# Kernel optimization log

Hardware: AMD Instinct MI355X
Metric: run time of the kernel (lower is better)

## Reference

```python
import jax, jax.numpy as jnp
import numpy as np

N = 50000      # num nodes
E = 800000     # num edges (no self loops; added in reference like add_remaining_self_loops)
D = 64         # input_dim
H = 128        # hidden_dim
O = 32         # output_dim
EPS = 1.0      # epsilon (privacy)
ALPHA = 0.5
DELTA = 1.0


def setup_inputs() -> dict:
    key = jax.random.key(0)
    ks = jax.random.split(key, 8)
    x = jax.random.normal(ks[0], (N, D), dtype=jnp.float32)
    row = jax.random.randint(ks[1], (E,), 0, N, dtype=jnp.int32)
    off = jax.random.randint(ks[2], (E,), 1, N, dtype=jnp.int32)
    col = (row + off) % N  # guarantees row != col (no pre-existing self loops)
    edge_index = jnp.stack([row, col], axis=0)
    priv_mask = jax.random.bernoulli(ks[3], 0.5, (N,))
    W1 = jax.random.normal(ks[4], (D, H), dtype=jnp.float32) * (1.0 / np.sqrt(D))
    b1 = jnp.zeros((H,), dtype=jnp.float32)
    W2 = jax.random.normal(ks[5], (H, O), dtype=jnp.float32) * (1.0 / np.sqrt(H))
    b2 = jnp.zeros((O,), dtype=jnp.float32)
    return {"x": x, "edge_index": edge_index, "priv_mask": priv_mask,
            "W1": W1, "b1": b1, "W2": W2, "b2": b2}


def _gcn_norm(edge_index, num_nodes, dtype):
    # add_remaining_self_loops + symmetric normalization deg^-1/2[row]*deg^-1/2[col]
    loops = jnp.arange(num_nodes, dtype=edge_index.dtype)
    row = jnp.concatenate([edge_index[0], loops])
    col = jnp.concatenate([edge_index[1], loops])
    deg = jax.ops.segment_sum(jnp.ones(row.shape[0], dtype=dtype), row,
                              num_segments=num_nodes)
    dis = deg ** -0.5  # deg >= 1 thanks to self loops
    norm = dis[row] * dis[col]  # [E+N]
    return row, col, norm


def reference(x, edge_index, priv_mask, W1, b1, W2, b2):
    row, col, norm = _gcn_norm(edge_index, N, x.dtype)
    exp_eps = float(np.exp(EPS))

    # ---- conv1 (GConvDP with per-node bool priv_mask) ----
    x_j = x[row]                                   # [E+N, D] gather
    p = priv_mask[row].astype(x.dtype)[:, None]    # [E+N, 1]
    transformed = ((exp_eps + 1.0) * x_j - 1.0) * (DELTA / (exp_eps - 1.0)) + ALPHA
    msg = norm[:, None] * (p * transformed + (1.0 - p) * x_j)
    h = jax.ops.segment_sum(msg, col, num_segments=N)  # scatter-add aggregate

    h = jax.nn.relu(h @ W1 + b1)
    # F.dropout skipped: reference is deterministic (eval mode)

    # ---- conv2 (called with priv_mask=False, a Python scalar) ----
    # Literal torch semantics: p_j = False -> False*(...) = 0, ~False = -1,
    # so msg = norm * (-x_j).
    msg2 = -norm[:, None] * h[row]                 # [E+N, H]
    h2 = jax.ops.segment_sum(msg2, col, num_segments=N)

    return h2 @ W2 + b2
```

## Files before the change

kernel.cpp:

```cpp
#include <hip/hip_runtime.h>
#include <math.h>

#define C1 2.163953413738653f
#define C0 -0.081976706869326f


static __device__ __forceinline__ unsigned short f2bf(float f) {
    unsigned b = __float_as_uint(f);
    return (unsigned short)((b + 0x7FFFu + ((b >> 16) & 1u)) >> 16);
}
static __device__ __forceinline__ float bf2f(unsigned short u) {
    return __uint_as_float((unsigned)u << 16);
}

__global__ __launch_bounds__(1024) void k_hist2(const int* __restrict__ row,
                                                const int* __restrict__ col, int E, int chunk,
                                                int* __restrict__ hist) {
    __shared__ int hc[256], hr[256];
    int t = threadIdx.x, b = blockIdx.x;
    if (t < 256) { hc[t] = 0; hr[t] = 0; }
    __syncthreads();
    int lo = b * chunk, hi = min(E, lo + chunk);
    for (int i = lo + t; i < hi; i += 1024) {
        atomicAdd(&hc[col[i] >> 8], 1);
        atomicAdd(&hr[row[i] >> 8], 1);
    }
    __syncthreads();
    if (t < 256) {
        hist[t * 256 + b] = hc[t];
        hist[65536 + t * 256 + b] = hr[t];
    }
}

__global__ void k_scan_a(const int* __restrict__ cnt, int* __restrict__ excl,
                         int* __restrict__ bsum, int n) {
    __shared__ int s[256];
    int idx = blockIdx.x * 256 + threadIdx.x;
    int v = (idx < n) ? cnt[idx] : 0;
    s[threadIdx.x] = v;
    __syncthreads();
    for (int off = 1; off < 256; off <<= 1) {
        int t = (threadIdx.x >= off) ? s[threadIdx.x - off] : 0;
        __syncthreads();
        s[threadIdx.x] += t;
        __syncthreads();
    }
    if (idx < n) excl[idx] = s[threadIdx.x] - v;
    if (threadIdx.x == 255) bsum[blockIdx.x] = s[255];
}

__global__ __launch_bounds__(512) void k_scan_bc(int* __restrict__ excl,
                                                 const int* __restrict__ bsum) {
    __shared__ int s[512];
    int t = threadIdx.x, b = blockIdx.x;
    s[t] = (t < b) ? bsum[t] : 0;
    __syncthreads();
    for (int off = 256; off > 0; off >>= 1) {
        if (t < off) s[t] += s[t + off];
        __syncthreads();
    }
    if (t < 256) excl[b * 256 + t] += s[0];
}

__global__ __launch_bounds__(1024) void k_part(const int* __restrict__ row,
                                               const int* __restrict__ col, int E, int chunk,
                                               const int* __restrict__ shist,
                                               unsigned* __restrict__ cbuf,
                                               unsigned short* __restrict__ rbuf) {
    __shared__ int offc[256], offr[256];
    int t = threadIdx.x, b = blockIdx.x;
    if (t < 256) {
        offc[t] = shist[t * 256 + b];
        offr[t] = shist[65536 + t * 256 + b] - E;
    }
    __syncthreads();
    int lo = b * chunk, hi = min(E, lo + chunk);
    for (int i = lo + t; i < hi; i += 1024) {
        int r = row[i], c = col[i];
        int pc = atomicAdd(&offc[c >> 8], 1);
        cbuf[pc] = ((unsigned)c << 16) | (unsigned)r;
        int pr = atomicAdd(&offr[r >> 8], 1);
        rbuf[pr] = (unsigned short)r;
    }
}

__global__ __launch_bounds__(256) void k_build(const unsigned short* __restrict__ rbuf,
                                               const unsigned* __restrict__ cbuf,
                                               const int* __restrict__ shist,
                                               const int* __restrict__ priv,
                                               const float* __restrict__ x, int N, int E, int nbk,
                                               float* __restrict__ dis,
                                               unsigned short* __restrict__ xt,
                                               int* __restrict__ cntC, int* __restrict__ colStart,
                                               unsigned short* __restrict__ eSrc) {
    __shared__ int s1[256], s2[256], s3[256];
    int t = threadIdx.x;
    if ((int)blockIdx.x < nbk) {
        int b = blockIdx.x;
        s1[t] = 0;
        __syncthreads();
        int rs = shist[65536 + b * 256] - E;
        int re = shist[65536 + (b + 1) * 256] - E;
        for (int i = rs + t; i < re; i += 256) atomicAdd(&s1[rbuf[i] & 255], 1);
        __syncthreads();
        int node = b * 256 + t;
        float dv = rsqrtf((float)(s1[t] + 1));
        if (node < N) {
            dis[node] = dv;
            s2[t] = __float_as_int(dv);
            s3[t] = priv[node];
        } else { s2[t] = 0; s3[t] = 0; }
        __syncthreads();
        int base = b * 256;
        for (int i = t; i < 256 * 16; i += 256) {
            int ln = i >> 4;
            int n2 = base + ln;
            if (n2 >= N) continue;
            float d2 = __int_as_float(s2[ln]);
            int p = s3[ln];
            float4 v = ((const float4*)x)[(size_t)n2 * 16 + (i & 15)];
            float4 tr;
            tr.x = p ? fmaf(C1, v.x, C0) : v.x;
            tr.y = p ? fmaf(C1, v.y, C0) : v.y;
            tr.z = p ? fmaf(C1, v.z, C0) : v.z;
            tr.w = p ? fmaf(C1, v.w, C0) : v.w;
            ushort4 o;
            o.x = f2bf(d2 * tr.x); o.y = f2bf(d2 * tr.y);
            o.z = f2bf(d2 * tr.z); o.w = f2bf(d2 * tr.w);
            ((ushort4*)xt)[(size_t)n2 * 16 + (i & 15)] = o;
        }
    } else {
        int b = blockIdx.x - nbk;
        s1[t] = 0; s3[t] = 0;
        __syncthreads();
        int cs = shist[b * 256];
        int ce = shist[(b + 1) * 256];
        for (int i = cs + t; i < ce; i += 256) atomicAdd(&s1[(cbuf[i] >> 16) & 255], 1);
        __syncthreads();
        int v = s1[t];
        s2[t] = v;
        __syncthreads();
        for (int off = 1; off < 256; off <<= 1) {
            int u = (t >= off) ? s2[t - off] : 0;
            __syncthreads();
            s2[t] += u;
            __syncthreads();
        }
        int excl = s2[t] - v;
        int c = b * 256 + t;
        if (c < N) { cntC[c] = v; colStart[c] = cs + excl; }
        __syncthreads();
        s2[t] = excl;
        __syncthreads();
        for (int i = cs + t; i < ce; i += 256) {
            unsigned e = cbuf[i];
            int d = (e >> 16) & 255;
            int pos = cs + s2[d] + atomicAdd(&s3[d], 1);
            eSrc[pos] = (unsigned short)(e & 0xFFFFu);
        }
    }
}

__global__ __launch_bounds__(256) void k_gather1(const unsigned short* __restrict__ xt,
                                                 const unsigned short* __restrict__ eSrc,
                                                 const int* __restrict__ colStart,
                                                 const int* __restrict__ cntC,
                                                 const float* __restrict__ dis,
                                                 unsigned short* __restrict__ agg1b, int N) {
    int t = blockIdx.x * blockDim.x + threadIdx.x;
    int c = t >> 6, d = t & 63;
    if (c >= N) return;
    float s = bf2f(xt[(size_t)c * 64 + d]);
    int start = colStart[c], cnt = cntC[c];
    for (int base = 0; base < cnt; base += 64) {
        int m = min(cnt - base, 64);
        int ids = (d < m) ? (int)eSrc[start + base + d] : 0;
        int k = 0;
        for (; k + 8 <= m; k += 8) {
            int r0 = __shfl(ids, k),     r1 = __shfl(ids, k + 1);
            int r2 = __shfl(ids, k + 2), r3 = __shfl(ids, k + 3);
            int r4 = __shfl(ids, k + 4), r5 = __shfl(ids, k + 5);
            int r6 = __shfl(ids, k + 6), r7 = __shfl(ids, k + 7);
            float x0 = bf2f(xt[(size_t)r0 * 64 + d]);
            float x1 = bf2f(xt[(size_t)r1 * 64 + d]);
            float x2 = bf2f(xt[(size_t)r2 * 64 + d]);
            float x3 = bf2f(xt[(size_t)r3 * 64 + d]);
            float x4 = bf2f(xt[(size_t)r4 * 64 + d]);
            float x5 = bf2f(xt[(size_t)r5 * 64 + d]);
            float x6 = bf2f(xt[(size_t)r6 * 64 + d]);
            float x7 = bf2f(xt[(size_t)r7 * 64 + d]);
            s += x0; s += x1; s += x2; s += x3;
            s += x4; s += x5; s += x6; s += x7;
        }
        for (; k + 4 <= m; k += 4) {
            int r0 = __shfl(ids, k),     r1 = __shfl(ids, k + 1);
            int r2 = __shfl(ids, k + 2), r3 = __shfl(ids, k + 3);
            float x0 = bf2f(xt[(size_t)r0 * 64 + d]);
            float x1 = bf2f(xt[(size_t)r1 * 64 + d]);
            float x2 = bf2f(xt[(size_t)r2 * 64 + d]);
            float x3 = bf2f(xt[(size_t)r3 * 64 + d]);
            s += x0; s += x1; s += x2; s += x3;
        }
        for (; k < m; ++k) {
            int r = __shfl(ids, k);
            s += bf2f(xt[(size_t)r * 64 + d]);
        }
    }
    agg1b[(size_t)c * 64 + d] = f2bf(dis[c] * s);
}

__global__ __launch_bounds__(256) void k_mlp_fused(const unsigned short* __restrict__ agg1b,
                                                   const float* __restrict__ W1,
                                                   const float* __restrict__ b1,
                                                   const float* __restrict__ W2,
                                                   const float* __restrict__ dis,
                                                   unsigned short* __restrict__ hps, int N) {
    __shared__ float hidT[128 * 68];
    __shared__ float W2s[128 * 32];
    float* As = hidT;
    const int t = threadIdx.x;
    const int base = blockIdx.x * 64;

    for (int i = t * 4; i < 128 * 32; i += 1024)
        *(float4*)&W2s[i] = *(const float4*)&W2[i];

    {
        int kq = t & 15, mm = t >> 4;
        #pragma unroll
        for (int p = 0; p < 4; ++p) {
            int m = mm + p * 16;
            int node = base + m;
            if (node >= N) node = N - 1;
            ushort4 v = ((const ushort4*)agg1b)[(size_t)node * 16 + kq];
            As[(kq * 4 + 0) * 68 + m] = bf2f(v.x);
            As[(kq * 4 + 1) * 68 + m] = bf2f(v.y);
            As[(kq * 4 + 2) * 68 + m] = bf2f(v.z);
            As[(kq * 4 + 3) * 68 + m] = bf2f(v.w);
        }
    }
    __syncthreads();

    const int tn = t & 31;
    const int tm = t >> 5;
    float4 bv = *(const float4*)&b1[tn * 4];
    float acc[8][4];
    #pragma unroll
    for (int i = 0; i < 8; ++i) {
        acc[i][0] = bv.x; acc[i][1] = bv.y; acc[i][2] = bv.z; acc[i][3] = bv.w;
    }
    #pragma unroll 4
    for (int k = 0; k < 64; ++k) {
        float4 w  = *(const float4*)&W1[k * 128 + tn * 4];
        float4 a0 = *(const float4*)&As[k * 68 + tm * 8];
        float4 a1 = *(const float4*)&As[k * 68 + tm * 8 + 4];
        const float av[8] = {a0.x, a0.y, a0.z, a0.w, a1.x, a1.y, a1.z, a1.w};
        #pragma unroll
        for (int i = 0; i < 8; ++i) {
            acc[i][0] = fmaf(av[i], w.x, acc[i][0]);
            acc[i][1] = fmaf(av[i], w.y, acc[i][1]);
            acc[i][2] = fmaf(av[i], w.z, acc[i][2]);
            acc[i][3] = fmaf(av[i], w.w, acc[i][3]);
        }
    }
    __syncthreads();

    #pragma unroll
    for (int j = 0; j < 4; ++j)
        #pragma unroll
        for (int i = 0; i < 8; ++i)
            hidT[(tn * 4 + j) * 68 + tm * 8 + i] = fmaxf(acc[i][j], 0.f);
    __syncthreads();

    const int to  = t & 15;
    const int tm2 = t >> 4;
    float o0[4] = {0.f, 0.f, 0.f, 0.f};
    float o1[4] = {0.f, 0.f, 0.f, 0.f};
    #pragma unroll 4
    for (int kh = 0; kh < 128; ++kh) {
        float4 a = *(const float4*)&hidT[kh * 68 + tm2 * 4];
        float2 w = *(const float2*)&W2s[kh * 32 + to * 2];
        const float av[4] = {a.x, a.y, a.z, a.w};
        #pragma unroll
        for (int i = 0; i < 4; ++i) {
            o0[i] = fmaf(av[i], w.x, o0[i]);
            o1[i] = fmaf(av[i], w.y, o1[i]);
        }
    }
    #pragma unroll
    for (int i = 0; i < 4; ++i) {
        int node = base + tm2 * 4 + i;
        if (node < N) {
            float dv = dis[node];
            ushort2 o = make_ushort2(f2bf(o0[i] * dv), f2bf(o1[i] * dv));
            *(ushort2*)&hps[(size_t)node * 32 + to * 2] = o;
        }
    }
}

__global__ __launch_bounds__(256) void k_gather2(const unsigned short* __restrict__ hps,
                                                 const unsigned short* __restrict__ eSrc,
                                                 const int* __restrict__ colStart,
                                                 const int* __restrict__ cntC,
                                                 const float* __restrict__ dis,
                                                 const float* __restrict__ b2,
                                                 float* __restrict__ out, int N) {
    int t = blockIdx.x * blockDim.x + threadIdx.x;
    int c = t >> 5, j = t & 31;
    if (c >= N) return;
    float s = bf2f(hps[(size_t)c * 32 + j]);
    int start = colStart[c], cnt = cntC[c];
    for (int base = 0; base < cnt; base += 32) {
        int m = min(cnt - base, 32);
        int ids = (j < m) ? (int)eSrc[start + base + j] : 0;
        int k = 0;
        for (; k + 8 <= m; k += 8) {
            int r0 = __shfl(ids, k, 32),     r1 = __shfl(ids, k + 1, 32);
            int r2 = __shfl(ids, k + 2, 32), r3 = __shfl(ids, k + 3, 32);
            int r4 = __shfl(ids, k + 4, 32), r5 = __shfl(ids, k + 5, 32);
            int r6 = __shfl(ids, k + 6, 32), r7 = __shfl(ids, k + 7, 32);
            float h0 = bf2f(hps[(size_t)r0 * 32 + j]);
            float h1 = bf2f(hps[(size_t)r1 * 32 + j]);
            float h2 = bf2f(hps[(size_t)r2 * 32 + j]);
            float h3 = bf2f(hps[(size_t)r3 * 32 + j]);
            float h4 = bf2f(hps[(size_t)r4 * 32 + j]);
            float h5 = bf2f(hps[(size_t)r5 * 32 + j]);
            float h6 = bf2f(hps[(size_t)r6 * 32 + j]);
            float h7 = bf2f(hps[(size_t)r7 * 32 + j]);
            s += h0; s += h1; s += h2; s += h3;
            s += h4; s += h5; s += h6; s += h7;
        }
        for (; k + 4 <= m; k += 4) {
            int r0 = __shfl(ids, k, 32),     r1 = __shfl(ids, k + 1, 32);
            int r2 = __shfl(ids, k + 2, 32), r3 = __shfl(ids, k + 3, 32);
            float h0 = bf2f(hps[(size_t)r0 * 32 + j]);
            float h1 = bf2f(hps[(size_t)r1 * 32 + j]);
            float h2 = bf2f(hps[(size_t)r2 * 32 + j]);
            float h3 = bf2f(hps[(size_t)r3 * 32 + j]);
            s += h0; s += h1; s += h2; s += h3;
        }
        for (; k < m; ++k) {
            int r = __shfl(ids, k, 32);
            s += bf2f(hps[(size_t)r * 32 + j]);
        }
    }
    out[(size_t)c * 32 + j] = b2[j] - dis[c] * s;
}

extern "C" void kernel_launch(void* const* d_in, const int* in_sizes, int n_in,
                              void* d_out, int out_size, void* d_ws, size_t ws_size,
                              hipStream_t stream) {
    const float* x    = (const float*)d_in[0];
    const int*   ei   = (const int*)d_in[1];
    const int*   priv = (const int*)d_in[2];
    const float* W1   = (const float*)d_in[3];
    const float* b1   = (const float*)d_in[4];
    const float* W2   = (const float*)d_in[5];
    const float* b2   = (const float*)d_in[6];
    float* out = (float*)d_out;

    const int N = in_sizes[2];
    const int E = in_sizes[1] / 2;
    const int* row = ei;
    const int* col = ei + E;

    char* ws = (char*)d_ws;
    size_t off = 0;
    auto take = [&](size_t bytes) { char* p = ws + off; off = (off + bytes + 255) & ~(size_t)255; return p; };
    int*            hist     = (int*)           take((size_t)131072 * 4);
    int*            shist    = (int*)           take((size_t)131072 * 4);
    int*            bsum     = (int*)           take(512 * 4);
    unsigned*       cbuf     = (unsigned*)      take((size_t)E * 4);
    unsigned short* rbuf     = (unsigned short*)take((size_t)E * 2);
    float*          dis      = (float*)         take((size_t)N * 4);
    int*            cntC     = (int*)           take((size_t)N * 4);
    int*            colStart = (int*)           take((size_t)N * 4);
    unsigned short* eSrc     = (unsigned short*)take((size_t)E * 2);
    unsigned short* xt       = (unsigned short*)take((size_t)N * 64 * 2);
    unsigned short* agg1b    = (unsigned short*)take((size_t)N * 64 * 2);
    unsigned short* hps      = (unsigned short*)take((size_t)N * 32 * 2);
    (void)ws_size;

    const int chunk = (E + 255) / 256;
    const int nbk = (N + 255) / 256;

    k_hist2    <<<256, 1024, 0, stream>>>(row, col, E, chunk, hist);
    k_scan_a   <<<512, 256, 0, stream>>>(hist, shist, bsum, 131072);
    k_scan_bc  <<<512, 512, 0, stream>>>(shist, bsum);
    k_part     <<<256, 1024, 0, stream>>>(row, col, E, chunk, shist, cbuf, rbuf);
    k_build    <<<2 * nbk, 256, 0, stream>>>(rbuf, cbuf, shist, priv, x, N, E, nbk,
                                             dis, xt, cntC, colStart, eSrc);
    k_gather1  <<<((size_t)N * 64 + 255) / 256, 256, 0, stream>>>(xt, eSrc, colStart, cntC, dis, agg1b, N);
    k_mlp_fused<<<(N + 63) / 64, 256, 0, stream>>>(agg1b, W1, b1, W2, dis, hps, N);
    k_gather2  <<<((size_t)N * 32 + 255) / 256, 256, 0, stream>>>(hps, eSrc, colStart, cntC, dis, b2, out, N);
}
```

Before: 175.8 us.

## Use bf16 MFMA for fused MLP and fold scan fixup into consumers

```diff
diff --git a/kernel.cpp b/kernel.cpp
--- a/kernel.cpp
+++ b/kernel.cpp
@@ -4,6 +4,9 @@
 #define C1 2.163953413738653f
 #define C0 -0.081976706869326f
 
+
+typedef __attribute__((ext_vector_type(8))) short bf16x8;
+typedef __attribute__((ext_vector_type(4))) float f32x4;
 
 static __device__ __forceinline__ unsigned short f2bf(float f) {
     unsigned b = __float_as_uint(f);
@@ -15,7 +18,11 @@
 
 __global__ __launch_bounds__(1024) void k_hist2(const int* __restrict__ row,
                                                 const int* __restrict__ col, int E, int chunk,
-                                                int* __restrict__ hist) {
+                                                int* __restrict__ hist,
+                                                const float* __restrict__ W1,
+                                                const float* __restrict__ W2,
+                                                unsigned short* __restrict__ W1b,
+                                                unsigned short* __restrict__ W2b) {
     __shared__ int hc[256], hr[256];
     int t = threadIdx.x, b = blockIdx.x;
     if (t < 256) { hc[t] = 0; hr[t] = 0; }
@@ -29,6 +36,19 @@
     if (t < 256) {
         hist[t * 256 + b] = hc[t];
         hist[65536 + t * 256 + b] = hr[t];
+    }
+    if (b == 0) {
+        for (int i = t; i < 8192; i += 1024) {
+            int j = i & 7, l2 = (i >> 3) & 63, kt = (i >> 9) & 1, nt = i >> 10;
+            int k = kt * 32 + (l2 >> 4) * 8 + j, n = nt * 16 + (l2 & 15);
+            W1b[i] = f2bf(W1[k * 128 + n]);
+        }
+    } else if (b == 1) {
+        for (int i = t; i < 4096; i += 1024) {
+            int j = i & 7, l2 = (i >> 3) & 63, kt = (i >> 9) & 3, nt = i >> 11;
+            int k = kt * 32 + (l2 >> 4) * 8 + j, n = nt * 16 + (l2 & 15);
+            W2b[i] = f2bf(W2[k * 32 + n]);
+        }
     }
 }
 
@@ -49,30 +69,33 @@
     if (threadIdx.x == 255) bsum[blockIdx.x] = s[255];
 }
 
-__global__ __launch_bounds__(512) void k_scan_bc(int* __restrict__ excl,
-                                                 const int* __restrict__ bsum) {
-    __shared__ int s[512];
-    int t = threadIdx.x, b = blockIdx.x;
-    s[t] = (t < b) ? bsum[t] : 0;
-    __syncthreads();
-    for (int off = 256; off > 0; off >>= 1) {
-        if (t < off) s[t] += s[t + off];
-        __syncthreads();
-    }
-    if (t < 256) excl[b * 256 + t] += s[0];
-}
-
 __global__ __launch_bounds__(1024) void k_part(const int* __restrict__ row,
                                                const int* __restrict__ col, int E, int chunk,
-                                               const int* __restrict__ shist,
+                                               const int* __restrict__ excl,
+                                               const int* __restrict__ bsum,
                                                unsigned* __restrict__ cbuf,
                                                unsigned short* __restrict__ rbuf) {
-    __shared__ int offc[256], offr[256];
+    __shared__ int offc[256], offr[256], s[256];
     int t = threadIdx.x, b = blockIdx.x;
-    if (t < 256) {
-        offc[t] = shist[t * 256 + b];
-        offr[t] = shist[65536 + t * 256 + b] - E;
-    }
+    if (t < 256) s[t] = bsum[t];
+    __syncthreads();
+    for (int off = 1; off < 256; off <<= 1) {
+        int u = (t < 256 && t >= off) ? s[t - off] : 0;
+        __syncthreads();
+        if (t < 256) s[t] += u;
+        __syncthreads();
+    }
+    if (t < 256) offc[t] = s[t] - bsum[t] + excl[t * 256 + b];
+    __syncthreads();
+    if (t < 256) s[t] = bsum[256 + t];
+    __syncthreads();
+    for (int off = 1; off < 256; off <<= 1) {
+        int u = (t < 256 && t >= off) ? s[t - off] : 0;
+        __syncthreads();
+        if (t < 256) s[t] += u;
+        __syncthreads();
+    }
+    if (t < 256) offr[t] = s[t] - bsum[256 + t] + excl[65536 + t * 256 + b];
     __syncthreads();
     int lo = b * chunk, hi = min(E, lo + chunk);
     for (int i = lo + t; i < hi; i += 1024) {
@@ -86,7 +109,7 @@
 
 __global__ __launch_bounds__(256) void k_build(const unsigned short* __restrict__ rbuf,
                                                const unsigned* __restrict__ cbuf,
-                                               const int* __restrict__ shist,
+                                               const int* __restrict__ bsum,
                                                const int* __restrict__ priv,
                                                const float* __restrict__ x, int N, int E, int nbk,
                                                float* __restrict__ dis,
@@ -97,10 +120,17 @@
     int t = threadIdx.x;
     if ((int)blockIdx.x < nbk) {
         int b = blockIdx.x;
+        s1[t] = (t < b) ? bsum[256 + t] : 0;
+        __syncthreads();
+        for (int off = 128; off > 0; off >>= 1) {
+            if (t < off) s1[t] += s1[t + off];
+            __syncthreads();
+        }
+        int rs = s1[0];
+        int re = rs + bsum[256 + b];
+        __syncthreads();
         s1[t] = 0;
         __syncthreads();
-        int rs = shist[65536 + b * 256] - E;
-        int re = shist[65536 + (b + 1) * 256] - E;
         for (int i = rs + t; i < re; i += 256) atomicAdd(&s1[rbuf[i] & 255], 1);
         __syncthreads();
         int node = b * 256 + t;
@@ -131,10 +161,17 @@
         }
     } else {
         int b = blockIdx.x - nbk;
+        s1[t] = (t < b) ? bsum[t] : 0;
+        __syncthreads();
+        for (int off = 128; off > 0; off >>= 1) {
+            if (t < off) s1[t] += s1[t + off];
+            __syncthreads();
+        }
+        int cs = s1[0];
+        int ce = cs + bsum[b];
+        __syncthreads();
         s1[t] = 0; s3[t] = 0;
         __syncthreads();
-        int cs = shist[b * 256];
-        int ce = shist[(b + 1) * 256];
         for (int i = cs + t; i < ce; i += 256) atomicAdd(&s1[(cbuf[i] >> 16) & 255], 1);
         __syncthreads();
         int v = s1[t];
@@ -209,90 +246,63 @@
     agg1b[(size_t)c * 64 + d] = f2bf(dis[c] * s);
 }
 
-__global__ __launch_bounds__(256) void k_mlp_fused(const unsigned short* __restrict__ agg1b,
-                                                   const float* __restrict__ W1,
-                                                   const float* __restrict__ b1,
-                                                   const float* __restrict__ W2,
-                                                   const float* __restrict__ dis,
-                                                   unsigned short* __restrict__ hps, int N) {
-    __shared__ float hidT[128 * 68];
-    __shared__ float W2s[128 * 32];
-    float* As = hidT;
+__global__ __launch_bounds__(256) void k_mlp_mfma(const unsigned short* __restrict__ agg1b,
+                                                  const unsigned short* __restrict__ W1b,
+                                                  const float* __restrict__ b1,
+                                                  const unsigned short* __restrict__ W2b,
+                                                  const float* __restrict__ dis,
+                                                  unsigned short* __restrict__ hps, int N) {
+    __shared__ unsigned short hidA[4][16 * 136];
     const int t = threadIdx.x;
-    const int base = blockIdx.x * 64;
-
-    for (int i = t * 4; i < 128 * 32; i += 1024)
-        *(float4*)&W2s[i] = *(const float4*)&W2[i];
-
+    const int w = t >> 6, l = t & 63;
+    const int q = l >> 4, lm = l & 15;
+    const int rowbase = blockIdx.x * 64 + w * 16;
+
+    bf16x8 a0, a1;
     {
-        int kq = t & 15, mm = t >> 4;
+        int node = rowbase + lm;
+        if (node >= N) node = N - 1;
+        const bf16x8* pa = (const bf16x8*)(agg1b + (size_t)node * 64);
+        a0 = pa[q];
+        a1 = pa[4 + q];
+    }
+    float dvals[4];
+    #pragma unroll
+    for (int r = 0; r < 4; ++r) {
+        int node = rowbase + q * 4 + r;
+        dvals[r] = (node < N) ? dis[node] : 0.f;
+    }
+
+    const bf16x8* w1f = (const bf16x8*)W1b;
+    #pragma unroll
+    for (int nt = 0; nt < 8; ++nt) {
+        float bv = b1[nt * 16 + lm];
+        f32x4 acc = {bv, bv, bv, bv};
+        acc = __builtin_amdgcn_mfma_f32_16x16x32_bf16(a0, w1f[(nt * 2 + 0) * 64 + l], acc, 0, 0, 0);
+        acc = __builtin_amdgcn_mfma_f32_16x16x32_bf16(a1, w1f[(nt * 2 + 1) * 64 + l], acc, 0, 0, 0);
         #pragma unroll
-        for (int p = 0; p < 4; ++p) {
-            int m = mm + p * 16;
-            int node = base + m;
-            if (node >= N) node = N - 1;
-            ushort4 v = ((const ushort4*)agg1b)[(size_t)node * 16 + kq];
-            As[(kq * 4 + 0) * 68 + m] = bf2f(v.x);
-            As[(kq * 4 + 1) * 68 + m] = bf2f(v.y);
-            As[(kq * 4 + 2) * 68 + m] = bf2f(v.z);
-            As[(kq * 4 + 3) * 68 + m] = bf2f(v.w);
-        }
-    }
-    __syncthreads();
-
-    const int tn = t & 31;
-    const int tm = t >> 5;
-    float4 bv = *(const float4*)&b1[tn * 4];
-    float acc[8][4];
+        for (int r = 0; r < 4; ++r)
+            hidA[w][(q * 4 + r) * 136 + nt * 16 + lm] = f2bf(fmaxf(acc[r], 0.f));
+    }
+    __syncthreads();
+
+    bf16x8 ha[4];
     #pragma unroll
-    for (int i = 0; i < 8; ++i) {
-        acc[i][0] = bv.x; acc[i][1] = bv.y; acc[i][2] = bv.z; acc[i][3] = bv.w;
-    }
-    #pragma unroll 4
-    for (int k = 0; k < 64; ++k) {
-        float4 w  = *(const float4*)&W1[k * 128 + tn * 4];
-        float4 a0 = *(const float4*)&As[k * 68 + tm * 8];
-        float4 a1 = *(const float4*)&As[k * 68 + tm * 8 + 4];
-        const float av[8] = {a0.x, a0.y, a0.z, a0.w, a1.x, a1.y, a1.z, a1.w};
+    for (int kt = 0; kt < 4; ++kt)
+        ha[kt] = *(const bf16x8*)&hidA[w][lm * 136 + kt * 32 + q * 8];
+
+    const bf16x8* w2f = (const bf16x8*)W2b;
+    #pragma unroll
+    for (int nt = 0; nt < 2; ++nt) {
+        f32x4 acc = {0.f, 0.f, 0.f, 0.f};
         #pragma unroll
-        for (int i = 0; i < 8; ++i) {
-            acc[i][0] = fmaf(av[i], w.x, acc[i][0]);
-            acc[i][1] = fmaf(av[i], w.y, acc[i][1]);
-            acc[i][2] = fmaf(av[i], w.z, acc[i][2]);
-            acc[i][3] = fmaf(av[i], w.w, acc[i][3]);
-        }
-    }
-    __syncthreads();
-
-    #pragma unroll
-    for (int j = 0; j < 4; ++j)
+        for (int kt = 0; kt < 4; ++kt)
+            acc = __builtin_amdgcn_mfma_f32_16x16x32_bf16(ha[kt], w2f[(nt * 4 + kt) * 64 + l], acc, 0, 0, 0);
         #pragma unroll
-        for (int i = 0; i < 8; ++i)
-            hidT[(tn * 4 + j) * 68 + tm * 8 + i] = fmaxf(acc[i][j], 0.f);
-    __syncthreads();
-
-    const int to  = t & 15;
-    const int tm2 = t >> 4;
-    float o0[4] = {0.f, 0.f, 0.f, 0.f};
-    float o1[4] = {0.f, 0.f, 0.f, 0.f};
-    #pragma unroll 4
-    for (int kh = 0; kh < 128; ++kh) {
-        float4 a = *(const float4*)&hidT[kh * 68 + tm2 * 4];
-        float2 w = *(const float2*)&W2s[kh * 32 + to * 2];
-        const float av[4] = {a.x, a.y, a.z, a.w};
-        #pragma unroll
-        for (int i = 0; i < 4; ++i) {
-            o0[i] = fmaf(av[i], w.x, o0[i]);
-            o1[i] = fmaf(av[i], w.y, o1[i]);
-        }
-    }
-    #pragma unroll
-    for (int i = 0; i < 4; ++i) {
-        int node = base + tm2 * 4 + i;
-        if (node < N) {
-            float dv = dis[node];
-            ushort2 o = make_ushort2(f2bf(o0[i] * dv), f2bf(o1[i] * dv));
-            *(ushort2*)&hps[(size_t)node * 32 + to * 2] = o;
+        for (int r = 0; r < 4; ++r) {
+            int node = rowbase + q * 4 + r;
+            if (node < N)
+                hps[(size_t)node * 32 + nt * 16 + lm] = f2bf(acc[r] * dvals[r]);
         }
     }
 }
@@ -367,8 +377,10 @@
     size_t off = 0;
     auto take = [&](size_t bytes) { char* p = ws + off; off = (off + bytes + 255) & ~(size_t)255; return p; };
     int*            hist     = (int*)           take((size_t)131072 * 4);
-    int*            shist    = (int*)           take((size_t)131072 * 4);
+    int*            excl     = (int*)           take((size_t)131072 * 4);
     int*            bsum     = (int*)           take(512 * 4);
+    unsigned short* W1b      = (unsigned short*)take((size_t)8192 * 2);
+    unsigned short* W2b      = (unsigned short*)take((size_t)4096 * 2);
     unsigned*       cbuf     = (unsigned*)      take((size_t)E * 4);
     unsigned short* rbuf     = (unsigned short*)take((size_t)E * 2);
     float*          dis      = (float*)         take((size_t)N * 4);
@@ -383,13 +395,12 @@
     const int chunk = (E + 255) / 256;
     const int nbk = (N + 255) / 256;
 
-    k_hist2    <<<256, 1024, 0, stream>>>(row, col, E, chunk, hist);
-    k_scan_a   <<<512, 256, 0, stream>>>(hist, shist, bsum, 131072);
-    k_scan_bc  <<<512, 512, 0, stream>>>(shist, bsum);
-    k_part     <<<256, 1024, 0, stream>>>(row, col, E, chunk, shist, cbuf, rbuf);
-    k_build    <<<2 * nbk, 256, 0, stream>>>(rbuf, cbuf, shist, priv, x, N, E, nbk,
-                                             dis, xt, cntC, colStart, eSrc);
-    k_gather1  <<<((size_t)N * 64 + 255) / 256, 256, 0, stream>>>(xt, eSrc, colStart, cntC, dis, agg1b, N);
-    k_mlp_fused<<<(N + 63) / 64, 256, 0, stream>>>(agg1b, W1, b1, W2, dis, hps, N);
-    k_gather2  <<<((size_t)N * 32 + 255) / 256, 256, 0, stream>>>(hps, eSrc, colStart, cntC, dis, b2, out, N);
-}
+    k_hist2   <<<256, 1024, 0, stream>>>(row, col, E, chunk, hist, W1, W2, W1b, W2b);
+    k_scan_a  <<<512, 256, 0, stream>>>(hist, excl, bsum, 131072);
+    k_part    <<<256, 1024, 0, stream>>>(row, col, E, chunk, excl, bsum, cbuf, rbuf);
+    k_build   <<<2 * nbk, 256, 0, stream>>>(rbuf, cbuf, bsum, priv, x, N, E, nbk,
+                                            dis, xt, cntC, colStart, eSrc);
+    k_gather1 <<<((size_t)N * 64 + 255) / 256, 256, 0, stream>>>(xt, eSrc, colStart, cntC, dis, agg1b, N);
+    k_mlp_mfma<<<(N + 63) / 64, 256, 0, stream>>>(agg1b, W1b, b1, W2b, dis, hps, N);
+    k_gather2 <<<((size_t)N * 32 + 255) / 256, 256, 0, stream>>>(hps, eSrc, colStart, cntC, dis, b2, out, N);
+}
```

Measured after the change: 157.9 us. 1.11x faster.
